# Kernel tuning notes

Measured on AMD Instinct MI355X. Metric: run time of the kernel, lower is better.

Reference implementation:

```python
import jax, jax.numpy as jnp
import numpy as np

NC = 512  # n_clusters (symbol alphabet size)
# (kernel, stride, padding) for each of the 17 symbolic conv layers
CFGS = [(7, 4, 0), (3, 1, 1), (3, 1, 1), (3, 1, 1), (3, 1, 1), (3, 2, 1),
        (3, 1, 1), (3, 1, 1), (3, 1, 1), (3, 2, 1), (3, 1, 1), (3, 1, 1),
        (3, 1, 1), (3, 2, 1), (3, 1, 1), (3, 1, 1), (3, 1, 1)]
RELU_AFTER = {0, 1, 3, 5, 7, 9, 11, 13, 15}
INS = [3, 64, 64, 64, 64, 64, 128, 128, 128, 128, 256, 256, 256, 256, 512, 512, 512]
OUTS = [64, 64, 64, 64, 64, 128, 128, 128, 128, 256, 256, 256, 256, 512, 512, 512, 512]


def setup_inputs() -> dict:
    key = jax.random.key(0)
    ks = jax.random.split(key, 26)
    inp = {"x": jax.random.normal(ks[0], (8, 3, 67, 67), dtype=jnp.float32)}
    for i in range(17):
        k = CFGS[i][0]
        inp[f"w{i}"] = jax.random.randint(ks[1 + i], (k * k * INS[i], OUTS[i]), 0, NC, dtype=jnp.int32)
    inp["conv_lut"] = jax.random.randint(ks[18], (NC, NC), 0, NC, dtype=jnp.int32)
    inp["add_lut"] = jax.random.randint(ks[19], (NC, NC), 0, NC, dtype=jnp.int32)
    inp["relu_lut"] = jax.random.randint(ks[20], (NC,), 0, NC, dtype=jnp.int32)
    inp["centroid_lut"] = jnp.sort(jax.random.normal(ks[21], (NC,), dtype=jnp.float32))
    inp["fc_w"] = jax.random.normal(ks[22], (1000, 512), dtype=jnp.float32) * 0.02
    inp["fc_b"] = jnp.zeros((1000,), dtype=jnp.float32)
    return inp


def _extract_patches(s, k, st):
    H, W, C = s.shape
    oh = (H - k) // st + 1
    ow = (W - k) // st + 1
    ri = (jnp.arange(oh) * st)[:, None] + jnp.arange(k)[None, :]  # (oh, k)
    ci = (jnp.arange(ow) * st)[:, None] + jnp.arange(k)[None, :]  # (ow, k)
    p = s[ri][:, :, ci]                      # (oh, k, ow, k, C)
    p = p.transpose(0, 2, 1, 3, 4)           # (oh, ow, k, k, C)
    return p.reshape(oh * ow, k * k * C), oh, ow


def _sym_conv(s, W, conv_lut, add_lut, k, st, pad):
    # LUT-based symbolic convolution: gather product symbols then fold the
    # window with the (non-associative) add_lut, exactly like functools.reduce.
    if pad:
        s = jnp.pad(s, ((pad, pad), (pad, pad), (0, 0)))
    pat, oh, ow = _extract_patches(s, k, st)
    m = conv_lut[pat[:, :, None], W[None, :, :]]
    def step(carry, row):                              # sequential LUT reduce over syms
        return add_lut[carry, row], None
    out, _ = jax.lax.scan(step, m[:, 0, :], jnp.moveaxis(m[:, 1:, :], 1, 0))
    return out.reshape(oh, ow, -1)


def reference(x, w0, w1, w2, w3, w4, w5, w6, w7, w8, w9, w10, w11, w12, w13,
              w14, w15, w16, conv_lut, add_lut, relu_lut, centroid_lut, fc_w, fc_b):
    ws = [w0, w1, w2, w3, w4, w5, w6, w7, w8, w9, w10, w11, w12, w13, w14, w15, w16]

    def per_image(img):                                 # img: (3, 67, 67)
        p = img.transpose(1, 2, 0)                      # (67, 67, 3)
        # discretize: nearest-centroid symbol per scalar (patch_size = 1x1)
        s = jnp.argmin((p[..., None] - centroid_lut) ** 2, axis=-1).astype(jnp.int32)
        for i, (k, st, pad) in enumerate(CFGS):
            s = _sym_conv(s, ws[i], conv_lut, add_lut, k, st, pad)
            if i in RELU_AFTER:
                s = relu_lut[s]
        vals = centroid_lut[s]                          # symbolic_to_image: (2, 2, 512)
        return jnp.mean(vals, axis=(0, 1))              # AdaptiveAvgPool2d((1,1)) -> (512,)

    feats = jax.vmap(per_image)(x)                      # (B, 512)
    return feats @ fc_w.T + fc_b                        # classifier: (B, 1000)
```

## Files before the change

### kernel.cpp

```cpp
#include <hip/hip_runtime.h>

typedef unsigned short u16;

#define NSYM 512

__global__ void build_tables_kernel(const int* __restrict__ conv_i,
                                    const int* __restrict__ add_i,
                                    const int* __restrict__ relu_i,
                                    u16* __restrict__ conv_u,
                                    u16* __restrict__ add_u,
                                    u16* __restrict__ addrelu_u) {
    int i = blockIdx.x * blockDim.x + threadIdx.x;
    if (i < NSYM * NSYM) {
        conv_u[i] = (u16)conv_i[i];
        int a = add_i[i];
        add_u[i] = (u16)a;
        addrelu_u[i] = (u16)relu_i[a];
    }
}

__global__ void quantize_kernel(const float* __restrict__ x,
                                u16* __restrict__ s0,
                                const float* __restrict__ cent,
                                int n) {
    __shared__ float c[NSYM];
    for (int t = threadIdx.x; t < NSYM; t += blockDim.x) c[t] = cent[t];
    __syncthreads();
    int i = blockIdx.x * blockDim.x + threadIdx.x;
    if (i >= n) return;
    int ch = i % 3; int t2 = i / 3; int xx = t2 % 67; int t3 = t2 / 67;
    int y = t3 % 67; int img = t3 / 67;
    float v = x[((img * 3 + ch) * 67 + y) * 67 + xx];
    int lo = 0, hi = NSYM;
    while (lo < hi) { int mid = (lo + hi) >> 1; if (c[mid] < v) lo = mid + 1; else hi = mid; }
    int idx;
    if (lo == 0) idx = 0;
    else if (lo == NSYM) idx = NSYM - 1;
    else {
        float d1 = v - c[lo - 1];
        float d2 = v - c[lo];
        idx = (d1 * d1 <= d2 * d2) ? (lo - 1) : lo;
    }
    s0[i] = (u16)idx;
}

__global__ __launch_bounds__(512) void symconv_ldsw_kernel(
        const u16* __restrict__ in, u16* __restrict__ out,
        const int* __restrict__ Wl,
        const u16* __restrict__ conv,
        const u16* __restrict__ addt,
        const u16* __restrict__ addlast,
        int H, int C, int OC, int nOCG,
        int K, int ST, int PAD, int OH, int OW, int PPB) {
    extern __shared__ u16 lds[];
    int J = K * K * C;
    u16* wlds = lds;
    u16* patch = lds + J * 64;

    int bid = blockIdx.x;
    int ocg = bid % nOCG;
    int pblk = bid / nOCG;
    int pixel0 = pblk * PPB;
    int tid = threadIdx.x;
    int nthr = PPB << 6;

    for (int t = tid; t < J * 64; t += nthr) {
        int j = t >> 6; int ocp = t & 63;
        wlds[t] = (u16)Wl[j * OC + (ocg << 6) + ocp];
    }
    for (int t = tid; t < PPB * J; t += nthr) {
        int p = t / J; int j = t - p * J;
        int c = j % C; int tt = j / C; int kc = tt % K; int kr = tt / K;
        int pix = pixel0 + p;
        int img = pix / (OH * OW); int rem = pix - img * (OH * OW);
        int oy = rem / OW; int ox = rem - oy * OW;
        int iy = oy * ST + kr - PAD;
        int ix = ox * ST + kc - PAD;
        u16 v = 0;
        if (iy >= 0 && iy < H && ix >= 0 && ix < H)
            v = in[((img * H + iy) * H + ix) * C + c];
        patch[p * J + j] = v;
    }
    __syncthreads();

    int wave = tid >> 6;
    int lane = tid & 63;
    int pix = pixel0 + wave;
    const u16* pat = patch + wave * J;

#define GM(j) ((int)conv[((int)pat[(j)] << 9) + (int)wlds[((j) << 6) + lane]])

    int carry = GM(0);
    int mA = GM(1);
    int mB = GM(2);
    int mC = GM(3);
    for (int j = 1; j < J - 3; ++j) {
        int mcur = mA; mA = mB; mB = mC;
        mC = GM(j + 3);
        carry = (int)addt[(carry << 9) + mcur];
    }
    carry = (int)addt[(carry << 9) + mA];
    carry = (int)addt[(carry << 9) + mB];
    carry = (int)addlast[(carry << 9) + mC];
    out[pix * OC + (ocg << 6) + lane] = (u16)carry;
#undef GM
}

__global__ __launch_bounds__(64) void symconv_glob_kernel(
        const u16* __restrict__ in, u16* __restrict__ out,
        const int* __restrict__ Wl,
        const u16* __restrict__ conv,
        const u16* __restrict__ addt,
        const u16* __restrict__ addlast,
        int H, int C, int OC, int nOCG,
        int K, int ST, int PAD, int OH, int OW) {
    extern __shared__ u16 patch[];
    int bid = blockIdx.x;
    int ocg = bid % nOCG;
    int pix = bid / nOCG;
    int img = pix / (OH * OW);
    int rem = pix - img * (OH * OW);
    int oy = rem / OW;
    int ox = rem - oy * OW;
    int J = K * K * C;
    for (int t = threadIdx.x; t < J; t += 64) {
        int c = t % C; int tt = t / C; int kc = tt % K; int kr = tt / K;
        int iy = oy * ST + kr - PAD;
        int ix = ox * ST + kc - PAD;
        u16 v = 0;
        if (iy >= 0 && iy < H && ix >= 0 && ix < H)
            v = in[((img * H + iy) * H + ix) * C + c];
        patch[t] = v;
    }
    __syncthreads();
    int oc = (ocg << 6) + threadIdx.x;

#define GM(j) ((int)conv[((int)patch[(j)] << 9) + Wl[(j) * OC + oc]])

    int carry = GM(0);
    int mA = GM(1);
    int mB = GM(2);
    int mC = GM(3);
    for (int j = 1; j < J - 3; ++j) {
        int mcur = mA; mA = mB; mB = mC;
        mC = GM(j + 3);
        carry = (int)addt[(carry << 9) + mcur];
    }
    carry = (int)addt[(carry << 9) + mA];
    carry = (int)addt[(carry << 9) + mB];
    carry = (int)addlast[(carry << 9) + mC];
    out[pix * OC + oc] = (u16)carry;
#undef GM
}

__global__ void head_kernel(const u16* __restrict__ s,
                            const float* __restrict__ cent,
                            const float* __restrict__ fcw,
                            const float* __restrict__ fcb,
                            float* __restrict__ out) {
    __shared__ float feats[NSYM];
    int img = blockIdx.x;
    const u16* sp = s + img * 4 * NSYM;
    for (int c = threadIdx.x; c < NSYM; c += blockDim.x) {
        float acc = cent[sp[c]] + cent[sp[NSYM + c]] +
                    cent[sp[2 * NSYM + c]] + cent[sp[3 * NSYM + c]];
        feats[c] = acc * 0.25f;
    }
    __syncthreads();
    int o = blockIdx.y * blockDim.x + threadIdx.x;
    if (o < 1000) {
        float acc = fcb[o];
        const float* wr = fcw + o * NSYM;
        for (int c2 = 0; c2 < NSYM; ++c2) acc += feats[c2] * wr[c2];
        out[img * 1000 + o] = acc;
    }
}

extern "C" void kernel_launch(void* const* d_in, const int* in_sizes, int n_in,
                              void* d_out, int out_size, void* d_ws, size_t ws_size,
                              hipStream_t stream) {
    const float* x = (const float*)d_in[0];
    const int* w[17];
    for (int i = 0; i < 17; ++i) w[i] = (const int*)d_in[1 + i];
    const int* conv_i = (const int*)d_in[18];
    const int* add_i  = (const int*)d_in[19];
    const int* relu_i = (const int*)d_in[20];
    const float* cent = (const float*)d_in[21];
    const float* fcw  = (const float*)d_in[22];
    const float* fcb  = (const float*)d_in[23];
    float* out = (float*)d_out;

    char* p = (char*)d_ws;
    u16* conv_u    = (u16*)p; p += NSYM * NSYM * 2;
    u16* add_u     = (u16*)p; p += NSYM * NSYM * 2;
    u16* addrelu_u = (u16*)p; p += NSYM * NSYM * 2;
    u16* act0      = (u16*)p; p += ((8 * 67 * 67 * 3 * 2 + 255) / 256) * 256;
    u16* actA      = (u16*)p; p += 8 * 16 * 16 * 64 * 2;
    u16* actB      = (u16*)p; p += 8 * 16 * 16 * 64 * 2;

    build_tables_kernel<<<(NSYM * NSYM + 255) / 256, 256, 0, stream>>>(
        conv_i, add_i, relu_i, conv_u, add_u, addrelu_u);

    int nq = 8 * 67 * 67 * 3;
    quantize_kernel<<<(nq + 255) / 256, 256, 0, stream>>>(x, act0, cent, nq);

    struct LC { int K, ST, PAD, C, OC, H, OH, relu, PPB; };
    static const LC L[17] = {
        {7,4,0,  3, 64,67,16,1, 8},
        {3,1,1, 64, 64,16,16,1, 8},
        {3,1,1, 64, 64,16,16,0, 8},
        {3,1,1, 64, 64,16,16,1, 8},
        {3,1,1, 64, 64,16,16,0, 8},
        {3,2,1, 64,128,16, 8,1, 4},
        {3,1,1,128,128, 8, 8,0, 4},
        {3,1,1,128,128, 8, 8,1, 4},
        {3,1,1,128,128, 8, 8,0, 4},
        {3,2,1,128,256, 8, 4,1, 2},
        {3,1,1,256,256, 4, 4,0, 0},
        {3,1,1,256,256, 4, 4,1, 0},
        {3,1,1,256,256, 4, 4,0, 0},
        {3,2,1,256,512, 4, 2,1, 0},
        {3,1,1,512,512, 2, 2,0, 0},
        {3,1,1,512,512, 2, 2,1, 0},
        {3,1,1,512,512, 2, 2,0, 0},
    };

    int maxlds = 0;
    for (int i = 0; i < 17; ++i) {
        if (L[i].PPB > 0) {
            int J = L[i].K * L[i].K * L[i].C;
            int b = J * 64 * 2 + L[i].PPB * J * 2;
            if (b > maxlds) maxlds = b;
        }
    }
    hipFuncSetAttribute((const void*)symconv_ldsw_kernel,
                        hipFuncAttributeMaxDynamicSharedMemorySize, maxlds);

    const u16* cur = act0;
    u16* nxt = actA;
    for (int i = 0; i < 17; ++i) {
        int OH = L[i].OH;
        int nOCG = L[i].OC / 64;
        int J = L[i].K * L[i].K * L[i].C;
        const u16* lastt = L[i].relu ? addrelu_u : add_u;
        if (L[i].PPB > 0) {
            int PPB = L[i].PPB;
            int pixels = 8 * OH * OH;
            int grid = (pixels / PPB) * nOCG;
            int ldsB = J * 64 * 2 + PPB * J * 2;
            symconv_ldsw_kernel<<<grid, PPB * 64, ldsB, stream>>>(
                cur, nxt, w[i], conv_u, add_u, lastt,
                L[i].H, L[i].C, L[i].OC, nOCG,
                L[i].K, L[i].ST, L[i].PAD, OH, OH, PPB);
        } else {
            int grid = 8 * OH * OH * nOCG;
            symconv_glob_kernel<<<grid, 64, J * 2, stream>>>(
                cur, nxt, w[i], conv_u, add_u, lastt,
                L[i].H, L[i].C, L[i].OC, nOCG,
                L[i].K, L[i].ST, L[i].PAD, OH, OH);
        }
        cur = nxt;
        nxt = (nxt == actA) ? actB : actA;
    }

    head_kernel<<<dim3(8, 4), 256, 0, stream>>>(cur, cent, fcw, fcb, out);
}
```

Baseline: 6.661 ms.

## Split deep-layer symbolic conv into producer/consumer waves with LDS double buffering

Removes the LDS-weight kernel and sends the early layers back to the one-wave-per-pixel global kernel. The deep layers (256/512 channels) get a new two-wave kernel: one wave gathers conv_lut products in chunks into a double-buffered LDS buffer, and the other runs the serial add_lut fold chain with pre-shifted byte offsets. The aim is to take the product-gather latency off the serial dependency chain. It costs block-wide barriers per chunk and gives up the weight reuse in LDS that the early layers had.

```diff
diff --git a/kernel.cpp b/kernel.cpp
--- a/kernel.cpp
+++ b/kernel.cpp
@@ -42,68 +42,6 @@
         idx = (d1 * d1 <= d2 * d2) ? (lo - 1) : lo;
     }
     s0[i] = (u16)idx;
-}
-
-__global__ __launch_bounds__(512) void symconv_ldsw_kernel(
-        const u16* __restrict__ in, u16* __restrict__ out,
-        const int* __restrict__ Wl,
-        const u16* __restrict__ conv,
-        const u16* __restrict__ addt,
-        const u16* __restrict__ addlast,
-        int H, int C, int OC, int nOCG,
-        int K, int ST, int PAD, int OH, int OW, int PPB) {
-    extern __shared__ u16 lds[];
-    int J = K * K * C;
-    u16* wlds = lds;
-    u16* patch = lds + J * 64;
-
-    int bid = blockIdx.x;
-    int ocg = bid % nOCG;
-    int pblk = bid / nOCG;
-    int pixel0 = pblk * PPB;
-    int tid = threadIdx.x;
-    int nthr = PPB << 6;
-
-    for (int t = tid; t < J * 64; t += nthr) {
-        int j = t >> 6; int ocp = t & 63;
-        wlds[t] = (u16)Wl[j * OC + (ocg << 6) + ocp];
-    }
-    for (int t = tid; t < PPB * J; t += nthr) {
-        int p = t / J; int j = t - p * J;
-        int c = j % C; int tt = j / C; int kc = tt % K; int kr = tt / K;
-        int pix = pixel0 + p;
-        int img = pix / (OH * OW); int rem = pix - img * (OH * OW);
-        int oy = rem / OW; int ox = rem - oy * OW;
-        int iy = oy * ST + kr - PAD;
-        int ix = ox * ST + kc - PAD;
-        u16 v = 0;
-        if (iy >= 0 && iy < H && ix >= 0 && ix < H)
-            v = in[((img * H + iy) * H + ix) * C + c];
-        patch[p * J + j] = v;
-    }
-    __syncthreads();
-
-    int wave = tid >> 6;
-    int lane = tid & 63;
-    int pix = pixel0 + wave;
-    const u16* pat = patch + wave * J;
-
-#define GM(j) ((int)conv[((int)pat[(j)] << 9) + (int)wlds[((j) << 6) + lane]])
-
-    int carry = GM(0);
-    int mA = GM(1);
-    int mB = GM(2);
-    int mC = GM(3);
-    for (int j = 1; j < J - 3; ++j) {
-        int mcur = mA; mA = mB; mB = mC;
-        mC = GM(j + 3);
-        carry = (int)addt[(carry << 9) + mcur];
-    }
-    carry = (int)addt[(carry << 9) + mA];
-    carry = (int)addt[(carry << 9) + mB];
-    carry = (int)addlast[(carry << 9) + mC];
-    out[pix * OC + (ocg << 6) + lane] = (u16)carry;
-#undef GM
 }
 
 __global__ __launch_bounds__(64) void symconv_glob_kernel(
@@ -153,6 +91,110 @@
 #undef GM
 }
 
+template <int DCH>
+__global__ __launch_bounds__(128) void symconv_deep_kernel(
+        const u16* __restrict__ in, u16* __restrict__ out,
+        const int* __restrict__ Wl,
+        const u16* __restrict__ conv,
+        const u16* __restrict__ addt,
+        const u16* __restrict__ addlast,
+        int H, int C, int OC, int nOCG,
+        int K, int ST, int PAD, int OH, int OW) {
+    extern __shared__ u16 lds[];
+    int J = K * K * C;
+    u16* patch = lds;
+    u16* mbuf = lds + J;
+
+    int bid = blockIdx.x;
+    int ocg = bid % nOCG;
+    int pix = bid / nOCG;
+    int img = pix / (OH * OW);
+    int rem = pix - img * (OH * OW);
+    int oy = rem / OW;
+    int ox = rem - oy * OW;
+    int tid = threadIdx.x;
+
+    for (int t = tid; t < J; t += 128) {
+        int c = t % C; int tt = t / C; int kc = tt % K; int kr = tt / K;
+        int iy = oy * ST + kr - PAD;
+        int ix = ox * ST + kc - PAD;
+        u16 v = 0;
+        if (iy >= 0 && iy < H && ix >= 0 && ix < H)
+            v = in[((img * H + iy) * H + ix) * C + c];
+        patch[t] = v;
+    }
+    __syncthreads();
+
+    int wave = tid >> 6;
+    int lane = tid & 63;
+    int oc = (ocg << 6) + lane;
+    int nch = J / DCH;
+
+    if (wave == 1) {
+        for (int t = 0; t < nch; ++t) {
+            u16* dst = mbuf + (t & 1) * (64 * DCH) + lane * DCH;
+            int j0 = t * DCH;
+            for (int k = 0; k < DCH; k += 8) {
+                int wv[8];
+                #pragma unroll
+                for (int u = 0; u < 8; ++u)
+                    wv[u] = Wl[(j0 + k + u) * OC + oc];
+                #pragma unroll
+                for (int u = 0; u < 8; ++u)
+                    dst[k + u] = (u16)(conv[((int)patch[j0 + k + u] << 9) + wv[u]] << 1);
+            }
+            __syncthreads();
+        }
+    } else {
+        unsigned carry = 0;
+        const char* ab = (const char*)addt;
+        for (int t = 0; t < nch; ++t) {
+            __syncthreads();
+            const u16* src = mbuf + (t & 1) * (64 * DCH) + lane * DCH;
+            bool lastchunk = (t == nch - 1);
+            int n2 = DCH - (lastchunk ? 1 : 0);
+            unsigned m2[8], m2n[8];
+            #pragma unroll
+            for (int u = 0; u < 8; ++u) m2[u] = src[u];
+            if (t == 0) {
+                carry = m2[0] >> 1;
+                #pragma unroll
+                for (int u = 1; u < 8; ++u) {
+                    unsigned off = (carry << 10) + m2[u];
+                    carry = *(const u16*)(ab + off);
+                }
+            } else {
+                #pragma unroll
+                for (int u = 0; u < 8; ++u) {
+                    unsigned off = (carry << 10) + m2[u];
+                    carry = *(const u16*)(ab + off);
+                }
+            }
+            for (int k = 8; k + 8 <= n2; k += 8) {
+                #pragma unroll
+                for (int u = 0; u < 8; ++u) m2n[u] = src[k + u];
+                #pragma unroll
+                for (int u = 0; u < 8; ++u) {
+                    unsigned off = (carry << 10) + m2n[u];
+                    carry = *(const u16*)(ab + off);
+                }
+            }
+            if (lastchunk) {
+                int k = (n2 / 8) * 8;
+                #pragma unroll
+                for (int u = 0; u < 8; ++u) m2n[u] = src[k + u];
+                #pragma unroll
+                for (int u = 0; u < 7; ++u) {
+                    unsigned off = (carry << 10) + m2n[u];
+                    carry = *(const u16*)(ab + off);
+                }
+                carry = addlast[(carry << 9) + (m2n[7] >> 1)];
+            }
+        }
+        out[pix * OC + oc] = (u16)carry;
+    }
+}
+
 __global__ void head_kernel(const u16* __restrict__ s,
                             const float* __restrict__ cent,
                             const float* __restrict__ fcw,
@@ -204,37 +246,42 @@
     int nq = 8 * 67 * 67 * 3;
     quantize_kernel<<<(nq + 255) / 256, 256, 0, stream>>>(x, act0, cent, nq);
 
-    struct LC { int K, ST, PAD, C, OC, H, OH, relu, PPB; };
+    struct LC { int K, ST, PAD, C, OC, H, OH, relu, deep; };
     static const LC L[17] = {
-        {7,4,0,  3, 64,67,16,1, 8},
-        {3,1,1, 64, 64,16,16,1, 8},
-        {3,1,1, 64, 64,16,16,0, 8},
-        {3,1,1, 64, 64,16,16,1, 8},
-        {3,1,1, 64, 64,16,16,0, 8},
-        {3,2,1, 64,128,16, 8,1, 4},
-        {3,1,1,128,128, 8, 8,0, 4},
-        {3,1,1,128,128, 8, 8,1, 4},
-        {3,1,1,128,128, 8, 8,0, 4},
-        {3,2,1,128,256, 8, 4,1, 2},
-        {3,1,1,256,256, 4, 4,0, 0},
-        {3,1,1,256,256, 4, 4,1, 0},
-        {3,1,1,256,256, 4, 4,0, 0},
-        {3,2,1,256,512, 4, 2,1, 0},
-        {3,1,1,512,512, 2, 2,0, 0},
-        {3,1,1,512,512, 2, 2,1, 0},
-        {3,1,1,512,512, 2, 2,0, 0},
+        {7,4,0,  3, 64,67,16,1, 0},
+        {3,1,1, 64, 64,16,16,1, 0},
+        {3,1,1, 64, 64,16,16,0, 0},
+        {3,1,1, 64, 64,16,16,1, 0},
+        {3,1,1, 64, 64,16,16,0, 0},
+        {3,2,1, 64,128,16, 8,1, 0},
+        {3,1,1,128,128, 8, 8,0, 0},
+        {3,1,1,128,128, 8, 8,1, 0},
+        {3,1,1,128,128, 8, 8,0, 0},
+        {3,2,1,128,256, 8, 4,1, 0},
+        {3,1,1,256,256, 4, 4,0, 1},
+        {3,1,1,256,256, 4, 4,1, 1},
+        {3,1,1,256,256, 4, 4,0, 1},
+        {3,2,1,256,512, 4, 2,1, 2},
+        {3,1,1,512,512, 2, 2,0, 2},
+        {3,1,1,512,512, 2, 2,1, 2},
+        {3,1,1,512,512, 2, 2,0, 2},
     };
 
-    int maxlds = 0;
+    int maxlds1 = 0, maxlds2 = 0;
     for (int i = 0; i < 17; ++i) {
-        if (L[i].PPB > 0) {
-            int J = L[i].K * L[i].K * L[i].C;
-            int b = J * 64 * 2 + L[i].PPB * J * 2;
-            if (b > maxlds) maxlds = b;
+        int J = L[i].K * L[i].K * L[i].C;
+        if (L[i].deep == 1) {
+            int b = J * 2 + 2 * 64 * 128 * 2;
+            if (b > maxlds1) maxlds1 = b;
+        } else if (L[i].deep == 2) {
+            int b = J * 2 + 2 * 64 * 256 * 2;
+            if (b > maxlds2) maxlds2 = b;
         }
     }
-    hipFuncSetAttribute((const void*)symconv_ldsw_kernel,
-                        hipFuncAttributeMaxDynamicSharedMemorySize, maxlds);
+    hipFuncSetAttribute((const void*)symconv_deep_kernel<128>,
+                        hipFuncAttributeMaxDynamicSharedMemorySize, maxlds1);
+    hipFuncSetAttribute((const void*)symconv_deep_kernel<256>,
+                        hipFuncAttributeMaxDynamicSharedMemorySize, maxlds2);
 
     const u16* cur = act0;
     u16* nxt = actA;
@@ -243,17 +290,20 @@
         int nOCG = L[i].OC / 64;
         int J = L[i].K * L[i].K * L[i].C;
         const u16* lastt = L[i].relu ? addrelu_u : add_u;
-        if (L[i].PPB > 0) {
-            int PPB = L[i].PPB;
-            int pixels = 8 * OH * OH;
-            int grid = (pixels / PPB) * nOCG;
-            int ldsB = J * 64 * 2 + PPB * J * 2;
-            symconv_ldsw_kernel<<<grid, PPB * 64, ldsB, stream>>>(
+        int grid = 8 * OH * OH * nOCG;
+        if (L[i].deep == 1) {
+            int ldsB = J * 2 + 2 * 64 * 128 * 2;
+            symconv_deep_kernel<128><<<grid, 128, ldsB, stream>>>(
                 cur, nxt, w[i], conv_u, add_u, lastt,
                 L[i].H, L[i].C, L[i].OC, nOCG,
-                L[i].K, L[i].ST, L[i].PAD, OH, OH, PPB);
+                L[i].K, L[i].ST, L[i].PAD, OH, OH);
+        } else if (L[i].deep == 2) {
+            int ldsB = J * 2 + 2 * 64 * 256 * 2;
+            symconv_deep_kernel<256><<<grid, 128, ldsB, stream>>>(
+                cur, nxt, w[i], conv_u, add_u, lastt,
+                L[i].H, L[i].C, L[i].OC, nOCG,
+                L[i].K, L[i].ST, L[i].PAD, OH, OH);
         } else {
-            int grid = 8 * OH * OH * nOCG;
             symconv_glob_kernel<<<grid, 64, J * 2, stream>>>(
                 cur, nxt, w[i], conv_u, add_u, lastt,
                 L[i].H, L[i].C, L[i].OC, nOCG,
```

Result: slower. 6.991 ms (+4.9%).
